# Kernel optimization log

Measured on AMD Instinct MI355X. Metric: run time of the kernel, lower is better.

## Reference

```python
import jax, jax.numpy as jnp
import numpy as np

B, N2, N3 = 16, 618, 2466
FEAT, HID, EMB = 963, 192, 8
IN_DIM = FEAT + HID + EMB  # 1163
N_BLOCKS, DEG = 6, 6
N_NEW = N3 - N2  # 1848


def setup_inputs() -> dict:
    key = jax.random.key(0)
    ks = jax.random.split(key, 24)
    rng = np.random.default_rng(0)
    # sparse-structured row-normalized adjacency on the 2466-vertex mesh
    nbrs = rng.integers(0, N3, size=(N3, DEG))
    A = np.zeros((N3, N3), np.float32)
    A[np.arange(N3)[:, None], nbrs] = 1.0 / DEG
    unpool_idx = jnp.asarray(rng.integers(0, N2, size=(N_NEW, 2)), dtype=jnp.int32)
    s = 0.05
    d = {
        "x": jax.random.normal(ks[0], (B, N2, FEAT), jnp.float32),
        "x2": jax.random.normal(ks[1], (B, N2, 3), jnp.float32),
        "x_hidden": jax.random.normal(ks[2], (B, N2, HID), jnp.float32),
        # GA self-attention projections over 8-dim multivectors
        "Wq": jax.random.normal(ks[3], (EMB, EMB), jnp.float32) * s,
        "bq": jnp.zeros((EMB,), jnp.float32),
        "Wk": jax.random.normal(ks[4], (EMB, EMB), jnp.float32) * s,
        "bk": jnp.zeros((EMB,), jnp.float32),
        "Wv": jax.random.normal(ks[5], (EMB, EMB), jnp.float32) * s,
        "bv": jnp.zeros((EMB,), jnp.float32),
        "adj": jnp.asarray(A),
        "unpool_idx": unpool_idx,
        # GBottleneck: entry GConv
        "W_in": jax.random.normal(ks[6], (IN_DIM, HID), jnp.float32) * s,
        "loopW_in": jax.random.normal(ks[7], (IN_DIM, HID), jnp.float32) * s,
        "b_in": jnp.zeros((HID,), jnp.float32),
        # 6 GResBlocks x 2 GConvs each
        "res_W": jax.random.normal(ks[8], (N_BLOCKS, 2, HID, HID), jnp.float32) * s,
        "res_loopW": jax.random.normal(ks[9], (N_BLOCKS, 2, HID, HID), jnp.float32) * s,
        "res_b": jnp.zeros((N_BLOCKS, 2, HID), jnp.float32),
        # GBottleneck exit GConv (hidden -> last_hidden_dim)
        "W_out": jax.random.normal(ks[10], (HID, HID), jnp.float32) * s,
        "loopW_out": jax.random.normal(ks[11], (HID, HID), jnp.float32) * s,
        "b_out": jnp.zeros((HID,), jnp.float32),
        # final GConv to coordinates
        "Wg": jax.random.normal(ks[12], (HID, 3), jnp.float32) * s,
        "loopWg": jax.random.normal(ks[13], (HID, 3), jnp.float32) * s,
        "bg": jnp.zeros((3,), jnp.float32),
    }
    return d


def _gconv(h, adj, W, loopW, b):
    # GConv: adj @ (h W) + h W_loop + b
    return jnp.einsum("mn,bnf->bmf", adj, h @ W) + h @ loopW + b


def reference(x, x2, x_hidden, Wq, bq, Wk, bk, Wv, bv, adj, unpool_idx,
              W_in, loopW_in, b_in, res_W, res_loopW, res_b,
              W_out, loopW_out, b_out, Wg, loopWg, bg):
    # embed coords as grade-1 part of Cl(3,0) multivector: [B,N2,8]
    mv = jnp.zeros(x2.shape[:2] + (EMB,), x2.dtype).at[..., 1:4].set(x2)
    q = mv @ Wq + bq
    k = mv @ Wk + bk
    v = mv @ Wv + bv
    attn = jax.nn.softmax(jnp.einsum("bnd,bmd->bnm", q, k) / jnp.sqrt(jnp.float32(EMB)), axis=-1)
    x2_att = jnp.einsum("bnm,bmd->bnd", attn, v)  # [B,N2,8]
    feat = jnp.concatenate([x, x_hidden, x2_att], axis=2)  # [B,N2,1163]
    # GUnpooling: new vertices = midpoint of the two parents
    new_v = 0.5 * (feat[:, unpool_idx[:, 0]] + feat[:, unpool_idx[:, 1]])
    h = jnp.concatenate([feat, new_v], axis=1)  # [B,N3,1163]
    # GBottleneck: entry conv + 6 residual blocks
    h = jax.nn.relu(_gconv(h, adj, W_in, loopW_in, b_in))
    for i in range(N_BLOCKS):
        y = jax.nn.relu(_gconv(h, adj, res_W[i, 0], res_loopW[i, 0], res_b[i, 0]))
        y = jax.nn.relu(_gconv(y, adj, res_W[i, 1], res_loopW[i, 1], res_b[i, 1]))
        h = 0.5 * (h + y)
    x4 = _gconv(h, adj, W_out, loopW_out, b_out)  # GBottleneck output head
    x4 = jax.nn.relu(x4)  # gconv_activation=True
    x4 = _gconv(x4, adj, Wg, loopWg, bg)  # [B,N3,3]
    return x4
```

## Files before the change

### kernel.cpp

```cpp
#include <hip/hip_runtime.h>
#include <hip/hip_bf16.h>

#define NB 16
#define N2V 618
#define N3V 2466
#define FEAT 963
#define HID 192
#define IN_DIM 1163
#define KPAD2 1216
#define ETILES 38
#define EHALF 19
#define MTOT (NB * N3V)
#define M2   (NB * N2V)

typedef __attribute__((ext_vector_type(8))) short bf16x8;
typedef __attribute__((ext_vector_type(4))) float f32x4;

__device__ __forceinline__ float bf2f(ushort u) {
    return __uint_as_float(((unsigned)u) << 16);
}
__device__ __forceinline__ ushort f2bf(float f) {
    unsigned u = __float_as_uint(f);
    return (ushort)((u + 0x7FFFu + ((u >> 16) & 1u)) >> 16);
}
__device__ __forceinline__ int xcd_swz(int bid, int G) {
    int q = G >> 3, r = G & 7;
    int xcd = bid & 7, slot = bid >> 3;
    return (xcd < r) ? xcd * (q + 1) + slot : r * (q + 1) + (xcd - r) * q + slot;
}

__global__ __launch_bounds__(256) void attn_fused(
    const float* __restrict__ x2,
    const float* __restrict__ Wq, const float* __restrict__ bq,
    const float* __restrict__ Wk, const float* __restrict__ bk,
    const float* __restrict__ Wv, const float* __restrict__ bv,
    float* __restrict__ att)
{
    __shared__ float4 kv[N2V * 4];
    int b = blockIdx.x, qb = blockIdx.y;
    const float* x2b = x2 + (size_t)b * N2V * 3;

    for (int i = threadIdx.x; i < N2V; i += 256) {
        float c0 = x2b[i * 3], c1 = x2b[i * 3 + 1], c2 = x2b[i * 3 + 2];
        float kk[8], vv[8];
#pragma unroll
        for (int d = 0; d < 8; ++d) {
            kk[d] = bk[d] + c0 * Wk[8 + d] + c1 * Wk[16 + d] + c2 * Wk[24 + d];
            vv[d] = bv[d] + c0 * Wv[8 + d] + c1 * Wv[16 + d] + c2 * Wv[24 + d];
        }
        kv[i * 2]     = (float4){kk[0], kk[1], kk[2], kk[3]};
        kv[i * 2 + 1] = (float4){kk[4], kk[5], kk[6], kk[7]};
        kv[N2V * 2 + i * 2]     = (float4){vv[0], vv[1], vv[2], vv[3]};
        kv[N2V * 2 + i * 2 + 1] = (float4){vv[4], vv[5], vv[6], vv[7]};
    }
    __syncthreads();

    int ql = threadIdx.x >> 4, sub = threadIdx.x & 15;
    int qi = qb * 16 + ql;
    bool valid = qi < N2V;
    float qv[8];
#pragma unroll
    for (int d = 0; d < 8; ++d) qv[d] = 0.f;
    if (valid) {
        float c0 = x2b[qi * 3], c1 = x2b[qi * 3 + 1], c2 = x2b[qi * 3 + 2];
#pragma unroll
        for (int d = 0; d < 8; ++d)
            qv[d] = bq[d] + c0 * Wq[8 + d] + c1 * Wq[16 + d] + c2 * Wq[24 + d];
    }

    const float scale = 0.35355339059327373f;
    float m = -3.0e38f, lsum = 0.f, acc[8];
#pragma unroll
    for (int d = 0; d < 8; ++d) acc[d] = 0.f;

    for (int kk = sub; kk < N2V; kk += 16) {
        float4 k0 = kv[kk * 2], k1 = kv[kk * 2 + 1];
        float s = qv[0] * k0.x + qv[1] * k0.y + qv[2] * k0.z + qv[3] * k0.w
                + qv[4] * k1.x + qv[5] * k1.y + qv[6] * k1.z + qv[7] * k1.w;
        s *= scale;
        float nm = fmaxf(m, s);
        float corr = __expf(m - nm);
        float p = __expf(s - nm);
        lsum = lsum * corr + p;
        float4 v0 = kv[N2V * 2 + kk * 2], v1 = kv[N2V * 2 + kk * 2 + 1];
        acc[0] = acc[0] * corr + p * v0.x; acc[1] = acc[1] * corr + p * v0.y;
        acc[2] = acc[2] * corr + p * v0.z; acc[3] = acc[3] * corr + p * v0.w;
        acc[4] = acc[4] * corr + p * v1.x; acc[5] = acc[5] * corr + p * v1.y;
        acc[6] = acc[6] * corr + p * v1.z; acc[7] = acc[7] * corr + p * v1.w;
        m = nm;
    }
#pragma unroll
    for (int o = 1; o <= 8; o <<= 1) {
        float m2 = __shfl_xor(m, o);
        float l2 = __shfl_xor(lsum, o);
        float nm = fmaxf(m, m2);
        float c1 = __expf(m - nm), c2 = __expf(m2 - nm);
        lsum = lsum * c1 + l2 * c2;
#pragma unroll
        for (int d = 0; d < 8; ++d) {
            float a2 = __shfl_xor(acc[d], o);
            acc[d] = acc[d] * c1 + a2 * c2;
        }
        m = nm;
    }
    if (valid && sub == 0) {
#pragma unroll
        for (int d = 0; d < 8; ++d)
            att[((size_t)b * N2V + qi) * 8 + d] = acc[d] / lsum;
    }
}

#define ENT_CHUNKS (24 * 38 * 64)
#define RES_CHUNKS (13 * 12 * 12 * 64)
#define WT_BLOCKS ((ENT_CHUNKS + RES_CHUNKS + 255) / 256)
__global__ void prep_all(const float* __restrict__ adj, const int* __restrict__ unpool,
                         int* __restrict__ cols, float* __restrict__ vals,
                         int* __restrict__ eidx, float* __restrict__ ew,
                         int* __restrict__ sidx,
                         const float* __restrict__ W_in, const float* __restrict__ loopW_in,
                         const float* __restrict__ res_W, const float* __restrict__ res_loopW,
                         const float* __restrict__ W_out, const float* __restrict__ loopW_out,
                         ushort* __restrict__ wt_e, ushort* __restrict__ wt_r)
{
    if (blockIdx.x >= N3V) {
        int idx = (blockIdx.x - N3V) * 256 + threadIdx.x;
        if (idx < ENT_CHUNKS) {
            int lane = idx & 63, r = idx >> 6;
            int kt = r % ETILES, ntile = r / ETILES;
            int n = ntile * 16 + (lane & 15);
            int k0 = kt * 32 + (lane >> 4) * 8;
            bf16x8 o;
#pragma unroll
            for (int j = 0; j < 8; ++j) {
                int k = k0 + j;
                float v = 0.f;
                if (k < IN_DIM) v = (n < 192) ? W_in[k * 192 + n] : loopW_in[k * 192 + (n - 192)];
                o[j] = (short)f2bf(v);
            }
            *(bf16x8*)(wt_e + (size_t)idx * 8) = o;
            return;
        }
        idx -= ENT_CHUNKS;
        if (idx >= RES_CHUNKS) return;
        int lane = idx & 63, r = idx >> 6;
        int kt = r % 12; r /= 12;
        int ntile = r % 12; int l = r / 12;
        const float* W = (l < 12) ? (res_W + (size_t)l * 192 * 192) : W_out;
        const float* L = (l < 12) ? (res_loopW + (size_t)l * 192 * 192) : loopW_out;
        int n = ntile * 16 + (lane & 15);
        int k0 = kt * 32 + (lane >> 4) * 8;
        bf16x8 o;
#pragma unroll
        for (int j = 0; j < 8; ++j) {
            int k2 = k0 + j;
            float v = (k2 < 192) ? W[k2 * 192 + n] : L[(k2 - 192) * 192 + n];
            o[j] = (short)f2bf(v);
        }
        *(bf16x8*)(wt_r + (size_t)idx * 8) = o;
        return;
    }

    int m = blockIdx.x;
    __shared__ int cnt;
    __shared__ int lc[8];
    __shared__ float lv[8];
    if (threadIdx.x == 0) cnt = 0;
    __syncthreads();
    for (int c = threadIdx.x; c < N3V; c += 256) {
        float a = adj[(size_t)m * N3V + c];
        if (a != 0.f) {
            int p = atomicAdd(&cnt, 1);
            if (p < 6) { lc[p] = c; lv[p] = a; }
        }
    }
    __syncthreads();
    if (threadIdx.x == 0) {
        int n = cnt < 6 ? cnt : 6;
        for (int i = 1; i < n; ++i) {
            int ci = lc[i]; float vi = lv[i]; int j = i - 1;
            while (j >= 0 && lc[j] > ci) { lc[j + 1] = lc[j]; lv[j + 1] = lv[j]; --j; }
            lc[j + 1] = ci; lv[j + 1] = vi;
        }
        int ne = 0;
        for (int i = 0; i < 6; ++i) {
            int c = (i < n) ? lc[i] : 0;
            float w = (i < n) ? lv[i] : 0.f;
            cols[m * 6 + i] = c;
            vals[m * 6 + i] = w;
            if (i < n) {
                if (c < N2V) { eidx[m * 12 + ne] = c; ew[m * 12 + ne] = w; ++ne; }
                else {
                    int jj = c - N2V;
                    eidx[m * 12 + ne] = unpool[2 * jj];     ew[m * 12 + ne] = 0.5f * w; ++ne;
                    eidx[m * 12 + ne] = unpool[2 * jj + 1]; ew[m * 12 + ne] = 0.5f * w; ++ne;
                }
            }
        }
        for (; ne < 12; ++ne) { eidx[m * 12 + ne] = 0; ew[m * 12 + ne] = 0.f; }
        if (m < N2V) { sidx[m * 2] = m; sidx[m * 2 + 1] = -1; }
        else {
            int j = m - N2V;
            sidx[m * 2] = unpool[2 * j];
            sidx[m * 2 + 1] = unpool[2 * j + 1];
        }
    }
}

__global__ void build_F3(const float* __restrict__ x, const float* __restrict__ xh,
                         const float* __restrict__ att, ushort* __restrict__ F3)
{
    int rt = blockIdx.x;
    for (int c = threadIdx.x; c < ETILES * 64; c += 256) {
        int kt = c >> 6, lane = c & 63;
        int row = rt * 16 + (lane & 15);
        int k0 = kt * 32 + (lane >> 4) * 8;
        bf16x8 o;
#pragma unroll
        for (int j = 0; j < 8; ++j) {
            int k = k0 + j;
            float v = 0.f;
            if (k < FEAT) v = x[(size_t)row * FEAT + k];
            else if (k < FEAT + HID) v = xh[(size_t)row * HID + (k - FEAT)];
            else if (k < IN_DIM) v = att[(size_t)row * 8 + (k - FEAT - HID)];
            o[j] = (short)f2bf(v);
        }
        *(bf16x8*)(F3 + ((size_t)(rt * ETILES + kt) * 64 + lane) * 8) = o;
    }
}

__global__ __launch_bounds__(512) void gemm_entry(
    const ushort* __restrict__ F3, const ushort* __restrict__ Wt,
    ushort* __restrict__ u2)
{
    __shared__ float part[64 * 192];

    int tid = threadIdx.x;
    int wave = tid >> 6, lane = tid & 63;
    int kh = wave >> 2, w4 = wave & 3;
    int lr = lane & 15, lkq = lane >> 4;
    int row0 = blockIdx.x * 64;
    int rt0 = blockIdx.x * 4;
    int lnb = w4 * 48;
    int nb = blockIdx.y * 192 + lnb;
    int ntile0 = nb >> 4;
    int tbeg = kh * EHALF, tend = tbeg + EHALF;

    int rts[4];
#pragma unroll
    for (int mt = 0; mt < 4; ++mt) {
        int rt = rt0 + mt;
        rts[mt] = (rt < M2 / 16) ? rt : (M2 / 16 - 1);
    }

    f32x4 acc[4][3];
#pragma unroll
    for (int mt = 0; mt < 4; ++mt)
#pragma unroll
        for (int nt = 0; nt < 3; ++nt) acc[mt][nt] = (f32x4){0.f, 0.f, 0.f, 0.f};

    bf16x8 a0[4], b0[3], a1[4], b1[3];
    auto LD = [&](int t, bf16x8 (&a)[4], bf16x8 (&b)[3]) {
#pragma unroll
        for (int mt = 0; mt < 4; ++mt)
            a[mt] = *(const bf16x8*)(F3 + ((size_t)(rts[mt] * ETILES + t) * 64 + lane) * 8);
#pragma unroll
        for (int nt = 0; nt < 3; ++nt)
            b[nt] = *(const bf16x8*)(Wt + ((size_t)((ntile0 + nt) * ETILES + t) * 64 + lane) * 8);
    };
    auto MM = [&](bf16x8 (&a)[4], bf16x8 (&b)[3]) {
#pragma unroll
        for (int mt = 0; mt < 4; ++mt)
#pragma unroll
            for (int nt = 0; nt < 3; ++nt)
                acc[mt][nt] = __builtin_amdgcn_mfma_f32_16x16x32_bf16(a[mt], b[nt], acc[mt][nt], 0, 0, 0);
    };

    LD(tbeg, a0, b0);
    for (int t = tbeg; t < tend; t += 2) {
        if (t + 1 < tend) LD(t + 1, a1, b1);
        MM(a0, b0);
        if (t + 2 < tend) LD(t + 2, a0, b0);
        if (t + 1 < tend) MM(a1, b1);
    }

    int crow = lkq * 4;
    if (kh == 1) {
#pragma unroll
        for (int mt = 0; mt < 4; ++mt)
#pragma unroll
            for (int r = 0; r < 4; ++r)
#pragma unroll
                for (int nt = 0; nt < 3; ++nt)
                    part[(mt * 16 + crow + r) * 192 + lnb + nt * 16 + lr] = acc[mt][nt][r];
    }
    __syncthreads();
    if (kh == 0) {
#pragma unroll
        for (int mt = 0; mt < 4; ++mt)
#pragma unroll
            for (int r = 0; r < 4; ++r) {
                int orow = row0 + mt * 16 + crow + r;
                if (orow < M2) {
#pragma unroll
                    for (int nt = 0; nt < 3; ++nt) {
                        float s = acc[mt][nt][r] + part[(mt * 16 + crow + r) * 192 + lnb + nt * 16 + lr];
                        u2[(size_t)orow * 384 + nb + nt * 16 + lr] = f2bf(s);
                    }
                }
            }
    }
}

__global__ void combine_entry(const ushort* __restrict__ u2, const int* __restrict__ eidx,
                              const float* __restrict__ ew, const int* __restrict__ sidx,
                              const float* __restrict__ bias, ushort* __restrict__ h)
{
    int lb = xcd_swz(blockIdx.x, gridDim.x);
    int tid = threadIdx.x;
    int rloc = tid / 24, f8 = tid % 24;
    int bm = lb * 8 + rloc;
    if (bm >= MTOT) return;
    int b = bm / N3V, n = bm % N3V;
    const ushort* base = u2 + (size_t)b * N2V * 384;

    float acc[8];
#pragma unroll
    for (int e = 0; e < 8; ++e) acc[e] = 0.f;
#pragma unroll
    for (int i = 0; i < 12; ++i) {
        float w = ew[n * 12 + i];
        bf16x8 v = *(const bf16x8*)(base + (size_t)eidx[n * 12 + i] * 384 + f8 * 8);
#pragma unroll
        for (int e = 0; e < 8; ++e) acc[e] += w * bf2f((ushort)v[e]);
    }
    int p0 = sidx[n * 2], p1 = sidx[n * 2 + 1];
    bf16x8 s0 = *(const bf16x8*)(base + (size_t)p0 * 384 + 192 + f8 * 8);
    if (p1 >= 0) {
        bf16x8 s1 = *(const bf16x8*)(base + (size_t)p1 * 384 + 192 + f8 * 8);
#pragma unroll
        for (int e = 0; e < 8; ++e) acc[e] += 0.5f * (bf2f((ushort)s0[e]) + bf2f((ushort)s1[e]));
    } else {
#pragma unroll
        for (int e = 0; e < 8; ++e) acc[e] += bf2f((ushort)s0[e]);
    }
    bf16x8 o;
#pragma unroll
    for (int e = 0; e < 8; ++e)
        o[e] = (short)f2bf(fmaxf(acc[e] + bias[f8 * 8 + e], 0.f));
    *(bf16x8*)(h + (size_t)bm * 192 + f8 * 8) = o;
}

template <int ACT>
__global__ __launch_bounds__(512) void gconv_fused(
    const ushort* __restrict__ src, const int* __restrict__ cols,
    const float* __restrict__ vals, const ushort* __restrict__ Wt,
    const float* __restrict__ bias, const ushort* __restrict__ hprev,
    ushort* __restrict__ outp)
{
    __shared__ ushort gs[32 * 192];
    __shared__ float part[32 * 192];

    int lb = xcd_swz(blockIdx.x, gridDim.x);
    int tid = threadIdx.x;
    int row0 = lb * 32;

    int wave = tid >> 6, lane = tid & 63;
    int kh = wave >> 2, w4 = wave & 3;
    int lr = lane & 15, lkq = lane >> 4, lk = lkq * 8;
    int nb = w4 * 48;
    int ntile0 = nb >> 4;
    int rows[2] = { row0 + lr, row0 + 16 + lr };
    int ktb = kh * 6;

    f32x4 acc[2][3];
#pragma unroll
    for (int mt = 0; mt < 2; ++mt)
#pragma unroll
        for (int nt = 0; nt < 3; ++nt) acc[mt][nt] = (f32x4){0.f, 0.f, 0.f, 0.f};

    bf16x8 a0[2], b0[3], a1[2], b1[3];
    auto LDself = [&](int t, bf16x8 (&a)[2], bf16x8 (&b)[3]) {
        int kk = t * 32 + lk;
#pragma unroll
        for (int mt = 0; mt < 2; ++mt)
            a[mt] = *(const bf16x8*)(src + (size_t)rows[mt] * 192 + kk);
#pragma unroll
        for (int nt = 0; nt < 3; ++nt)
            b[nt] = *(const bf16x8*)(Wt + ((size_t)((ntile0 + nt) * 12 + ktb + t) * 64 + lane) * 8);
    };
    auto LDg = [&](int t, bf16x8 (&a)[2], bf16x8 (&b)[3]) {
#pragma unroll
        for (int mt = 0; mt < 2; ++mt) {
            int rr = mt * 16 + lr;
            int byte = rr * 384 + t * 64 + lkq * 16;
            byte ^= (rr & 7) << 4;
            a[mt] = *(const bf16x8*)((const char*)gs + byte);
        }
#pragma unroll
        for (int nt = 0; nt < 3; ++nt)
            b[nt] = *(const bf16x8*)(Wt + ((size_t)((ntile0 + nt) * 12 + ktb + t) * 64 + lane) * 8);
    };
    auto MM = [&](bf16x8 (&a)[2], bf16x8 (&b)[3]) {
#pragma unroll
        for (int mt = 0; mt < 2; ++mt)
#pragma unroll
            for (int nt = 0; nt < 3; ++nt)
                acc[mt][nt] = __builtin_amdgcn_mfma_f32_16x16x32_bf16(a[mt], b[nt], acc[mt][nt], 0, 0, 0);
    };

    int crow = lkq * 4;

    if (kh == 1) {
        LDself(0, a0, b0);
#pragma unroll
        for (int t = 0; t < 6; t += 2) {
            if (t + 1 < 6) LDself(t + 1, a1, b1);
            MM(a0, b0);
            if (t + 2 < 6) LDself(t + 2, a0, b0);
            if (t + 1 < 6) MM(a1, b1);
        }
#pragma unroll
        for (int mt = 0; mt < 2; ++mt)
#pragma unroll
            for (int r = 0; r < 4; ++r)
#pragma unroll
                for (int nt = 0; nt < 3; ++nt)
                    part[(mt * 16 + crow + r) * 192 + nb + nt * 16 + lr] = acc[mt][nt][r];
    } else {
#pragma unroll
        for (int it = 0; it < 3; ++it) {
            int task = tid + it * 256;
            int r = task / 24, f8 = task % 24;
            int bm = row0 + r;
            int b = bm / N3V, m = bm % N3V;
            const ushort* hb = src + (size_t)b * N3V * 192;
            float ga[8];
#pragma unroll
            for (int e = 0; e < 8; ++e) ga[e] = 0.f;
#pragma unroll
            for (int j = 0; j < 6; ++j) {
                float w = vals[m * 6 + j];
                bf16x8 v = *(const bf16x8*)(hb + (size_t)cols[m * 6 + j] * 192 + f8 * 8);
#pragma unroll
                for (int e = 0; e < 8; ++e) ga[e] += w * bf2f((ushort)v[e]);
            }
            bf16x8 o;
#pragma unroll
            for (int e = 0; e < 8; ++e) o[e] = (short)f2bf(ga[e]);
            int byte = r * 384 + f8 * 16;
            byte ^= (r & 7) << 4;
            *(bf16x8*)((char*)gs + byte) = o;
        }
    }
    __syncthreads();

    if (kh == 0) {
        LDg(0, a0, b0);
#pragma unroll
        for (int t = 0; t < 6; t += 2) {
            if (t + 1 < 6) LDg(t + 1, a1, b1);
            MM(a0, b0);
            if (t + 2 < 6) LDg(t + 2, a0, b0);
            if (t + 1 < 6) MM(a1, b1);
        }
#pragma unroll
        for (int mt = 0; mt < 2; ++mt)
#pragma unroll
            for (int r = 0; r < 4; ++r) {
                int orow = row0 + mt * 16 + crow + r;
#pragma unroll
                for (int nt = 0; nt < 3; ++nt) {
                    int nn = nb + nt * 16 + lr;
                    float s = acc[mt][nt][r] + part[(mt * 16 + crow + r) * 192 + nn] + bias[nn];
                    s = fmaxf(s, 0.f);
                    if (ACT) s = 0.5f * (bf2f(hprev[(size_t)orow * 192 + nn]) + s);
                    outp[(size_t)orow * 192 + nn] = f2bf(s);
                }
            }
    }
}

__global__ void head_a2(const ushort* __restrict__ y, const float* __restrict__ Wg,
                        const float* __restrict__ loopWg, float* __restrict__ t)
{
    int tid = threadIdx.x;
    int rloc = tid >> 2, sub = tid & 3;
    int bm = blockIdx.x * 64 + rloc;
    if (bm >= MTOT) return;
    float s[6];
#pragma unroll
    for (int c = 0; c < 6; ++c) s[c] = 0.f;
#pragma unroll
    for (int kk = 0; kk < 6; ++kk) {
        int kg = sub * 6 + kk;
        bf16x8 v = *(const bf16x8*)(y + (size_t)bm * 192 + kg * 8);
#pragma unroll
        for (int e = 0; e < 8; ++e) {
            float f = bf2f((ushort)v[e]);
            int k = kg * 8 + e;
            s[0] += f * Wg[k * 3 + 0];
            s[1] += f * Wg[k * 3 + 1];
            s[2] += f * Wg[k * 3 + 2];
            s[3] += f * loopWg[k * 3 + 0];
            s[4] += f * loopWg[k * 3 + 1];
            s[5] += f * loopWg[k * 3 + 2];
        }
    }
#pragma unroll
    for (int o = 1; o <= 2; o <<= 1)
#pragma unroll
        for (int c = 0; c < 6; ++c) s[c] += __shfl_xor(s[c], o);
    if (sub == 0) {
#pragma unroll
        for (int c = 0; c < 6; ++c) t[(size_t)bm * 6 + c] = s[c];
    }
}

__global__ void head_b(const float* __restrict__ t, const int* __restrict__ cols,
                       const float* __restrict__ vals, const float* __restrict__ bg,
                       float* __restrict__ out)
{
    int idx = blockIdx.x * 256 + threadIdx.x;
    if (idx >= MTOT * 3) return;
    int bm = idx / 3, c = idx % 3;
    int b = bm / N3V, m = bm % N3V;
    float s = 0.f;
#pragma unroll
    for (int j = 0; j < 6; ++j)
        s += vals[m * 6 + j] * t[((size_t)b * N3V + cols[m * 6 + j]) * 6 + c];
    s += t[(size_t)bm * 6 + 3 + c] + bg[c];
    out[idx] = s;
}

extern "C" void kernel_launch(void* const* d_in, const int* in_sizes, int n_in,
                              void* d_out, int out_size, void* d_ws, size_t ws_size,
                              hipStream_t stream)
{
    const float* x        = (const float*)d_in[0];
    const float* x2       = (const float*)d_in[1];
    const float* xh       = (const float*)d_in[2];
    const float* Wq       = (const float*)d_in[3];
    const float* bq       = (const float*)d_in[4];
    const float* Wk       = (const float*)d_in[5];
    const float* bk       = (const float*)d_in[6];
    const float* Wv       = (const float*)d_in[7];
    const float* bv       = (const float*)d_in[8];
    const float* adj      = (const float*)d_in[9];
    const int*   unpool   = (const int*)d_in[10];
    const float* W_in     = (const float*)d_in[11];
    const float* loopW_in = (const float*)d_in[12];
    const float* b_in     = (const float*)d_in[13];
    const float* res_W    = (const float*)d_in[14];
    const float* res_loopW= (const float*)d_in[15];
    const float* res_b    = (const float*)d_in[16];
    const float* W_out    = (const float*)d_in[17];
    const float* loopW_out= (const float*)d_in[18];
    const float* b_out    = (const float*)d_in[19];
    const float* Wg       = (const float*)d_in[20];
    const float* loopWg   = (const float*)d_in[21];
    const float* bg       = (const float*)d_in[22];
    float* out = (float*)d_out;

    char* ws = (char*)d_ws;
    size_t o = 0;
    auto alloc = [&](size_t bytes) { char* p = ws + o; o += (bytes + 255) & ~(size_t)255; return p; };
    float*  att  = (float*)alloc((size_t)M2 * 8 * 4);
    int*    cols = (int*)alloc((size_t)N3V * 6 * 4);
    float*  vals = (float*)alloc((size_t)N3V * 6 * 4);
    int*    eidx = (int*)alloc((size_t)N3V * 12 * 4);
    float*  ewgt = (float*)alloc((size_t)N3V * 12 * 4);
    int*    sidx = (int*)alloc((size_t)N3V * 2 * 4);
    ushort* F3   = (ushort*)alloc((size_t)M2 * KPAD2 * 2);
    ushort* wt_e = (ushort*)alloc((size_t)ENT_CHUNKS * 8 * 2);
    ushort* wt_r = (ushort*)alloc((size_t)RES_CHUNKS * 8 * 2);
    ushort* u2   = (ushort*)alloc((size_t)M2 * 384 * 2);
    ushort* h    = (ushort*)alloc((size_t)MTOT * 192 * 2);
    ushort* h2   = (ushort*)alloc((size_t)MTOT * 192 * 2);
    ushort* y    = (ushort*)alloc((size_t)MTOT * 192 * 2);
    float*  ts   = (float*)alloc((size_t)MTOT * 6 * 4);
    if (ws_size < o) return;

    attn_fused<<<dim3(NB, 39), 256, 0, stream>>>(x2, Wq, bq, Wk, bk, Wv, bv, att);
    prep_all<<<N3V + WT_BLOCKS, 256, 0, stream>>>(adj, unpool, cols, vals, eidx, ewgt, sidx,
        W_in, loopW_in, res_W, res_loopW, W_out, loopW_out, wt_e, wt_r);
    build_F3<<<M2 / 16, 256, 0, stream>>>(x, xh, att, F3);

    gemm_entry<<<dim3((M2 + 63) / 64, 2), 512, 0, stream>>>(F3, wt_e, u2);
    combine_entry<<<(MTOT + 7) / 8, 192, 0, stream>>>(u2, eidx, ewgt, sidx, b_in, h);

    int gg = MTOT / 32;
    ushort* cur = h;
    ushort* nxt = h2;
    for (int i = 0; i < 6; ++i) {
        const float* B0 = res_b + (size_t)(i * 2 + 0) * 192;
        const float* B1 = res_b + (size_t)(i * 2 + 1) * 192;
        const ushort* W0 = wt_r + (size_t)(i * 2 + 0) * (12 * 12 * 64 * 8);
        const ushort* W1 = wt_r + (size_t)(i * 2 + 1) * (12 * 12 * 64 * 8);
        gconv_fused<0><<<gg, 512, 0, stream>>>(cur, cols, vals, W0, B0, nullptr, y);
        gconv_fused<1><<<gg, 512, 0, stream>>>(y, cols, vals, W1, B1, cur, nxt);
        ushort* tmp = cur; cur = nxt; nxt = tmp;
    }

    gconv_fused<0><<<gg, 512, 0, stream>>>(cur, cols, vals,
        wt_r + (size_t)12 * (12 * 12 * 64 * 8), b_out, nullptr, y);

    head_a2<<<(MTOT + 63) / 64, 256, 0, stream>>>(y, Wg, loopWg, ts);
    head_b<<<(MTOT * 3 + 255) / 256, 256, 0, stream>>>(ts, cols, vals, bg, out);
}
```

Measured before the change: 412.3 us.

## Split aggregated GEMM across all waves and fuse final head kernels

In gconv_fused, the second phase (the GEMM on the gathered neighbour aggregate) now runs on all 8 waves, each taking 16 rows, where before only 4 waves did it over 32 rows while the other 4 sat idle. This halves the per-wave MFMA chain after the barrier. The two-kernel coordinate head, which wrote an intermediate buffer, becomes one kernel that recomputes each neighbour's projection from y. That removes a launch and the intermediate round trip but does six times more projection arithmetic and reads of neighbour rows.

After: 453.9 us. +10.1%, slower.

```diff
diff --git a/kernel.cpp b/kernel.cpp
--- a/kernel.cpp
+++ b/kernel.cpp
@@ -365,59 +365,44 @@
     int row0 = lb * 32;
 
     int wave = tid >> 6, lane = tid & 63;
-    int kh = wave >> 2, w4 = wave & 3;
+    int w4 = wave & 3, wm = wave >> 2;
     int lr = lane & 15, lkq = lane >> 4, lk = lkq * 8;
     int nb = w4 * 48;
     int ntile0 = nb >> 4;
-    int rows[2] = { row0 + lr, row0 + 16 + lr };
-    int ktb = kh * 6;
-
-    f32x4 acc[2][3];
-#pragma unroll
-    for (int mt = 0; mt < 2; ++mt)
-#pragma unroll
-        for (int nt = 0; nt < 3; ++nt) acc[mt][nt] = (f32x4){0.f, 0.f, 0.f, 0.f};
-
-    bf16x8 a0[2], b0[3], a1[2], b1[3];
-    auto LDself = [&](int t, bf16x8 (&a)[2], bf16x8 (&b)[3]) {
-        int kk = t * 32 + lk;
+    int crow = lkq * 4;
+
+    if (wave >= 4) {
+        int rows[2] = { row0 + lr, row0 + 16 + lr };
+        f32x4 acc[2][3];
 #pragma unroll
         for (int mt = 0; mt < 2; ++mt)
-            a[mt] = *(const bf16x8*)(src + (size_t)rows[mt] * 192 + kk);
-#pragma unroll
-        for (int nt = 0; nt < 3; ++nt)
-            b[nt] = *(const bf16x8*)(Wt + ((size_t)((ntile0 + nt) * 12 + ktb + t) * 64 + lane) * 8);
-    };
-    auto LDg = [&](int t, bf16x8 (&a)[2], bf16x8 (&b)[3]) {
-#pragma unroll
-        for (int mt = 0; mt < 2; ++mt) {
-            int rr = mt * 16 + lr;
-            int byte = rr * 384 + t * 64 + lkq * 16;
-            byte ^= (rr & 7) << 4;
-            a[mt] = *(const bf16x8*)((const char*)gs + byte);
-        }
-#pragma unroll
-        for (int nt = 0; nt < 3; ++nt)
-            b[nt] = *(const bf16x8*)(Wt + ((size_t)((ntile0 + nt) * 12 + ktb + t) * 64 + lane) * 8);
-    };
-    auto MM = [&](bf16x8 (&a)[2], bf16x8 (&b)[3]) {
-#pragma unroll
-        for (int mt = 0; mt < 2; ++mt)
+#pragma unroll
+            for (int nt = 0; nt < 3; ++nt) acc[mt][nt] = (f32x4){0.f, 0.f, 0.f, 0.f};
+
+        bf16x8 a0[2], b0[3], a1[2], b1[3];
+        auto LDs = [&](int t, bf16x8 (&a)[2], bf16x8 (&b)[3]) {
+            int kk = t * 32 + lk;
+#pragma unroll
+            for (int mt = 0; mt < 2; ++mt)
+                a[mt] = *(const bf16x8*)(src + (size_t)rows[mt] * 192 + kk);
 #pragma unroll
             for (int nt = 0; nt < 3; ++nt)
-                acc[mt][nt] = __builtin_amdgcn_mfma_f32_16x16x32_bf16(a[mt], b[nt], acc[mt][nt], 0, 0, 0);
-    };
-
-    int crow = lkq * 4;
-
-    if (kh == 1) {
-        LDself(0, a0, b0);
+                b[nt] = *(const bf16x8*)(Wt + ((size_t)((ntile0 + nt) * 12 + 6 + t) * 64 + lane) * 8);
+        };
+        auto MMs = [&](bf16x8 (&a)[2], bf16x8 (&b)[3]) {
+#pragma unroll
+            for (int mt = 0; mt < 2; ++mt)
+#pragma unroll
+                for (int nt = 0; nt < 3; ++nt)
+                    acc[mt][nt] = __builtin_amdgcn_mfma_f32_16x16x32_bf16(a[mt], b[nt], acc[mt][nt], 0, 0, 0);
+        };
+        LDs(0, a0, b0);
 #pragma unroll
         for (int t = 0; t < 6; t += 2) {
-            if (t + 1 < 6) LDself(t + 1, a1, b1);
-            MM(a0, b0);
-            if (t + 2 < 6) LDself(t + 2, a0, b0);
-            if (t + 1 < 6) MM(a1, b1);
+            if (t + 1 < 6) LDs(t + 1, a1, b1);
+            MMs(a0, b0);
+            if (t + 2 < 6) LDs(t + 2, a0, b0);
+            if (t + 1 < 6) MMs(a1, b1);
         }
 #pragma unroll
         for (int mt = 0; mt < 2; ++mt)
@@ -454,82 +439,104 @@
     }
     __syncthreads();
 
-    if (kh == 0) {
+    {
+        f32x4 acc2[3];
+#pragma unroll
+        for (int nt = 0; nt < 3; ++nt) acc2[nt] = (f32x4){0.f, 0.f, 0.f, 0.f};
+
+        bf16x8 a0, b0[3], a1, b1[3];
+        auto LDg = [&](int t, bf16x8 &a, bf16x8 (&b)[3]) {
+            int rr = wm * 16 + lr;
+            int byte = rr * 384 + t * 64 + lkq * 16;
+            byte ^= (rr & 7) << 4;
+            a = *(const bf16x8*)((const char*)gs + byte);
+#pragma unroll
+            for (int nt = 0; nt < 3; ++nt)
+                b[nt] = *(const bf16x8*)(Wt + ((size_t)((ntile0 + nt) * 12 + t) * 64 + lane) * 8);
+        };
+        auto MMg = [&](bf16x8 &a, bf16x8 (&b)[3]) {
+#pragma unroll
+            for (int nt = 0; nt < 3; ++nt)
+                acc2[nt] = __builtin_amdgcn_mfma_f32_16x16x32_bf16(a, b[nt], acc2[nt], 0, 0, 0);
+        };
         LDg(0, a0, b0);
 #pragma unroll
         for (int t = 0; t < 6; t += 2) {
             if (t + 1 < 6) LDg(t + 1, a1, b1);
-            MM(a0, b0);
+            MMg(a0, b0);
             if (t + 2 < 6) LDg(t + 2, a0, b0);
-            if (t + 1 < 6) MM(a1, b1);
-        }
-#pragma unroll
-        for (int mt = 0; mt < 2; ++mt)
-#pragma unroll
-            for (int r = 0; r < 4; ++r) {
-                int orow = row0 + mt * 16 + crow + r;
-#pragma unroll
-                for (int nt = 0; nt < 3; ++nt) {
-                    int nn = nb + nt * 16 + lr;
-                    float s = acc[mt][nt][r] + part[(mt * 16 + crow + r) * 192 + nn] + bias[nn];
-                    s = fmaxf(s, 0.f);
-                    if (ACT) s = 0.5f * (bf2f(hprev[(size_t)orow * 192 + nn]) + s);
-                    outp[(size_t)orow * 192 + nn] = f2bf(s);
-                }
+            if (t + 1 < 6) MMg(a1, b1);
+        }
+
+#pragma unroll
+        for (int r = 0; r < 4; ++r) {
+            int orow = row0 + wm * 16 + crow + r;
+#pragma unroll
+            for (int nt = 0; nt < 3; ++nt) {
+                int nn = nb + nt * 16 + lr;
+                float s = acc2[nt][r] + part[(wm * 16 + crow + r) * 192 + nn] + bias[nn];
+                s = fmaxf(s, 0.f);
+                if (ACT) s = 0.5f * (bf2f(hprev[(size_t)orow * 192 + nn]) + s);
+                outp[(size_t)orow * 192 + nn] = f2bf(s);
             }
-    }
-}
-
-__global__ void head_a2(const ushort* __restrict__ y, const float* __restrict__ Wg,
-                        const float* __restrict__ loopWg, float* __restrict__ t)
+        }
+    }
+}
+
+__global__ void head_fused(const ushort* __restrict__ y, const int* __restrict__ cols,
+                           const float* __restrict__ vals, const float* __restrict__ Wg,
+                           const float* __restrict__ loopWg, const float* __restrict__ bg,
+                           float* __restrict__ out)
 {
     int tid = threadIdx.x;
     int rloc = tid >> 2, sub = tid & 3;
     int bm = blockIdx.x * 64 + rloc;
     if (bm >= MTOT) return;
-    float s[6];
-#pragma unroll
-    for (int c = 0; c < 6; ++c) s[c] = 0.f;
+    int b = bm / N3V, m = bm % N3V;
+    const ushort* yb = y + (size_t)b * N3V * 192;
+
+    float s[3] = {0.f, 0.f, 0.f};
 #pragma unroll
     for (int kk = 0; kk < 6; ++kk) {
         int kg = sub * 6 + kk;
-        bf16x8 v = *(const bf16x8*)(y + (size_t)bm * 192 + kg * 8);
+        bf16x8 v = *(const bf16x8*)(yb + (size_t)m * 192 + kg * 8);
 #pragma unroll
         for (int e = 0; e < 8; ++e) {
             float f = bf2f((ushort)v[e]);
             int k = kg * 8 + e;
-            s[0] += f * Wg[k * 3 + 0];
-            s[1] += f * Wg[k * 3 + 1];
-            s[2] += f * Wg[k * 3 + 2];
-            s[3] += f * loopWg[k * 3 + 0];
-            s[4] += f * loopWg[k * 3 + 1];
-            s[5] += f * loopWg[k * 3 + 2];
-        }
+            s[0] += f * loopWg[k * 3 + 0];
+            s[1] += f * loopWg[k * 3 + 1];
+            s[2] += f * loopWg[k * 3 + 2];
+        }
+    }
+#pragma unroll
+    for (int j = 0; j < 6; ++j) {
+        float w = vals[m * 6 + j];
+        const ushort* yr = yb + (size_t)cols[m * 6 + j] * 192;
+        float t0 = 0.f, t1 = 0.f, t2 = 0.f;
+#pragma unroll
+        for (int kk = 0; kk < 6; ++kk) {
+            int kg = sub * 6 + kk;
+            bf16x8 v = *(const bf16x8*)(yr + kg * 8);
+#pragma unroll
+            for (int e = 0; e < 8; ++e) {
+                float f = bf2f((ushort)v[e]);
+                int k = kg * 8 + e;
+                t0 += f * Wg[k * 3 + 0];
+                t1 += f * Wg[k * 3 + 1];
+                t2 += f * Wg[k * 3 + 2];
+            }
+        }
+        s[0] += w * t0; s[1] += w * t1; s[2] += w * t2;
     }
 #pragma unroll
     for (int o = 1; o <= 2; o <<= 1)
 #pragma unroll
-        for (int c = 0; c < 6; ++c) s[c] += __shfl_xor(s[c], o);
+        for (int c = 0; c < 3; ++c) s[c] += __shfl_xor(s[c], o);
     if (sub == 0) {
 #pragma unroll
-        for (int c = 0; c < 6; ++c) t[(size_t)bm * 6 + c] = s[c];
-    }
-}
-
-__global__ void head_b(const float* __restrict__ t, const int* __restrict__ cols,
-                       const float* __restrict__ vals, const float* __restrict__ bg,
-                       float* __restrict__ out)
-{
-    int idx = blockIdx.x * 256 + threadIdx.x;
-    if (idx >= MTOT * 3) return;
-    int bm = idx / 3, c = idx % 3;
-    int b = bm / N3V, m = bm % N3V;
-    float s = 0.f;
-#pragma unroll
-    for (int j = 0; j < 6; ++j)
-        s += vals[m * 6 + j] * t[((size_t)b * N3V + cols[m * 6 + j]) * 6 + c];
-    s += t[(size_t)bm * 6 + 3 + c] + bg[c];
-    out[idx] = s;
+        for (int c = 0; c < 3; ++c) out[(size_t)bm * 3 + c] = s[c] + bg[c];
+    }
 }
 
 extern "C" void kernel_launch(void* const* d_in, const int* in_sizes, int n_in,
@@ -577,7 +584,6 @@
     ushort* h    = (ushort*)alloc((size_t)MTOT * 192 * 2);
     ushort* h2   = (ushort*)alloc((size_t)MTOT * 192 * 2);
     ushort* y    = (ushort*)alloc((size_t)MTOT * 192 * 2);
-    float*  ts   = (float*)alloc((size_t)MTOT * 6 * 4);
     if (ws_size < o) return;
 
     attn_fused<<<dim3(NB, 39), 256, 0, stream>>>(x2, Wq, bq, Wk, bk, Wv, bv, att);
@@ -604,6 +610,5 @@
     gconv_fused<0><<<gg, 512, 0, stream>>>(cur, cols, vals,
         wt_r + (size_t)12 * (12 * 12 * 64 * 8), b_out, nullptr, y);
 
-    head_a2<<<(MTOT + 63) / 64, 256, 0, stream>>>(y, Wg, loopWg, ts);
-    head_b<<<(MTOT * 3 + 255) / 256, 256, 0, stream>>>(ts, cols, vals, bg, out);
-}
+    head_fused<<<(MTOT + 63) / 64, 256, 0, stream>>>(y, cols, vals, Wg, loopWg, bg, out);
+}
```
